# Performance work log

Hardware: AMD Instinct MI355X
Metric: run time of the kernel (lower is better)

Reference implementation:

```python
import jax, jax.numpy as jnp
import numpy as np

NUM_HEADS = 16
THETA = 10000.0


def _rope(x, pos, theta):
    # x: [B, H, S, D], pos: [S] ints. Interleaved-pair RoPE.
    D = x.shape[-1]
    half = D // 2
    inv_freq = theta ** (-(jnp.arange(half, dtype=jnp.float32) * 2.0) / D)  # [half]
    ang = pos.astype(jnp.float32)[:, None] * inv_freq[None, :]              # [S, half]
    cos, sin = jnp.cos(ang), jnp.sin(ang)
    x1 = x[..., 0::2]
    x2 = x[..., 1::2]
    r1 = x1 * cos - x2 * sin
    r2 = x1 * sin + x2 * cos
    return jnp.stack([r1, r2], axis=-1).reshape(x.shape)


def setup_inputs() -> dict:
    key = jax.random.key(0)
    ks = jax.random.split(key, 5)
    B, S, D = 4, 2048, 1024
    scale = 1.0 / np.sqrt(D)
    x = jax.random.normal(ks[0], (B, S, D), dtype=jnp.float32)
    Wq = jax.random.normal(ks[1], (D, D), dtype=jnp.float32) * scale
    Wk = jax.random.normal(ks[2], (D, D), dtype=jnp.float32) * scale
    Wv = jax.random.normal(ks[3], (D, D), dtype=jnp.float32) * scale
    Wo = jax.random.normal(ks[4], (D, D), dtype=jnp.float32) * scale
    token_positions = jnp.arange(S, dtype=jnp.int64)
    return {"x": x, "Wq": Wq, "Wk": Wk, "Wv": Wv, "Wo": Wo,
            "token_positions": token_positions}


def reference(x, Wq, Wk, Wv, Wo, token_positions):
    B, S, D = x.shape
    H = NUM_HEADS
    hd = D // H
    # Projections (weights stored as [d_model, d_k], matching the transposed params)
    q = jnp.einsum('bsd,de->bse', x, Wq).reshape(B, S, H, hd).transpose(0, 2, 1, 3)
    k = jnp.einsum('bsd,de->bse', x, Wk).reshape(B, S, H, hd).transpose(0, 2, 1, 3)
    v = jnp.einsum('bsd,de->bse', x, Wv).reshape(B, S, H, hd).transpose(0, 2, 1, 3)
    # RoPE on q and k
    q = _rope(q, token_positions, THETA)
    k = _rope(k, token_positions, THETA)
    # Causal scaled dot-product attention
    scores = jnp.einsum('bhqd,bhkd->bhqk', q, k) / jnp.sqrt(jnp.float32(hd))
    causal = jnp.tril(jnp.ones((S, S), dtype=bool))
    scores = jnp.where(causal, scores, jnp.float32(-jnp.inf))
    attn = jax.nn.softmax(scores, axis=-1)
    o = jnp.einsum('bhqk,bhkd->bhqd', attn, v)          # [B, H, S, hd]
    o = o.transpose(0, 2, 1, 3).reshape(B, S, D)         # [B, S, D]
    return jnp.einsum('bsd,de->bse', o, Wo)
```

## Files before the change

### kernel.cpp

```cpp
#include <hip/hip_runtime.h>
#include <math.h>

#define B_ 4
#define S_ 2048
#define D_ 1024
#define H_ 16
#define HD_ 64
#define ES_F 0.180336880111f
#define KF (-0.41524101186f)

typedef unsigned short ushort_t;
typedef __attribute__((ext_vector_type(8))) short short8;
typedef __attribute__((ext_vector_type(4))) short short4_t;
typedef __attribute__((ext_vector_type(4))) float f32x4;
typedef __attribute__((ext_vector_type(16))) float f32x16;
typedef __attribute__((ext_vector_type(2))) unsigned uint2v;

typedef const void __attribute__((address_space(1))) gvoid;
typedef void __attribute__((address_space(3))) lvoid;

__device__ __forceinline__ ushort_t f2bf(float f) {
    union { float f; unsigned u; } v; v.f = f;
    unsigned r = (v.u + 0x7FFFu + ((v.u >> 16) & 1u)) >> 16;
    return (ushort_t)r;
}
__device__ __forceinline__ float fexp2(float x) {
#if __has_builtin(__builtin_amdgcn_exp2f)
    return __builtin_amdgcn_exp2f(x);
#else
    return exp2f(x);
#endif
}
__device__ __forceinline__ unsigned pk2t(float a, float b) {
    union { float f; unsigned u; } A, Bv; A.f = a; Bv.f = b;
#if __has_builtin(__builtin_amdgcn_perm)
    return __builtin_amdgcn_perm(Bv.u, A.u, 0x07060302u);
#else
    return (A.u >> 16) | (Bv.u & 0xFFFF0000u);
#endif
}
__device__ __forceinline__ short8 mk_frag(unsigned a, unsigned b, unsigned c, unsigned d) {
    union { unsigned u[4]; short8 s; } t;
    t.u[0] = a; t.u[1] = b; t.u[2] = c; t.u[3] = d; return t.s;
}

__global__ __launch_bounds__(256)
void cvt_all(const float* __restrict__ x, ushort_t* __restrict__ xb,
             const float* __restrict__ W0, const float* __restrict__ W1,
             const float* __restrict__ W2, const float* __restrict__ W3,
             ushort_t* __restrict__ T0, ushort_t* __restrict__ T1,
             ushort_t* __restrict__ T2, ushort_t* __restrict__ T3)
{
    __shared__ __align__(16) float T[64 * 68];
    const int bx = blockIdx.x;
    const int t = threadIdx.x;

    if (bx < 4096) {
        const size_t i = ((size_t)bx * 256 + t) * 8;
        float4 a = *(const float4*)&x[i];
        float4 b = *(const float4*)&x[i + 4];
        short8 o;
        o[0] = (short)f2bf(a.x); o[1] = (short)f2bf(a.y);
        o[2] = (short)f2bf(a.z); o[3] = (short)f2bf(a.w);
        o[4] = (short)f2bf(b.x); o[5] = (short)f2bf(b.y);
        o[6] = (short)f2bf(b.z); o[7] = (short)f2bf(b.w);
        *(short8*)&xb[i] = o;
        return;
    }

    const int id = bx - 4096;
    const int z = id >> 8;
    const float* W = (z == 0) ? W0 : (z == 1) ? W1 : (z == 2) ? W2 : W3;
    ushort_t* Wt = (z == 0) ? T0 : (z == 1) ? T1 : (z == 2) ? T2 : T3;
    const int n0 = (id & 15) * 64, k0 = ((id >> 4) & 15) * 64;

    const int row = t >> 2, c0 = (t & 3) * 16;
#pragma unroll
    for (int u = 0; u < 4; ++u)
        *(float4*)&T[row * 68 + c0 + u * 4] =
            *(const float4*)&W[(size_t)(k0 + row) * D_ + n0 + c0 + u * 4];
    __syncthreads();
    const int n = t >> 2, kc = (t & 3) * 16;
    short8 o0, o1;
#pragma unroll
    for (int kk = 0; kk < 8; ++kk) o0[kk] = (short)f2bf(T[(kc + kk) * 68 + n]);
#pragma unroll
    for (int kk = 0; kk < 8; ++kk) o1[kk] = (short)f2bf(T[(kc + 8 + kk) * 68 + n]);
    *(short8*)&Wt[(size_t)(n0 + n) * D_ + k0 + kc] = o0;
    *(short8*)&Wt[(size_t)(n0 + n) * D_ + k0 + kc + 8] = o1;
}


#define QSTAGE(tt, src, base, dst) {                                           \
    const int kk_ = (tt) * 64;                                                 \
    _Pragma("unroll") for (int i_ = 0; i_ < 4; ++i_) {                         \
        const int rb_ = (i_ * 4 + w) * 8;                                      \
        __builtin_amdgcn_global_load_lds(                                      \
            (gvoid*)&(src)[(size_t)((base) + rb_ + srow) * D_ + kk_ + sch],    \
            (lvoid*)&(dst)[rb_ * 64], 16, 0, 0);                               \
    } }

__global__ __launch_bounds__(256, 2)
void qkv_fused(const ushort_t* __restrict__ A,
               const ushort_t* __restrict__ Wq, const ushort_t* __restrict__ Wk,
               const ushort_t* __restrict__ Wv,
               ushort_t* __restrict__ dQ, ushort_t* __restrict__ dK,
               ushort_t* __restrict__ dV)
{
    __shared__ __align__(16) ushort_t Xs[128 * 64];
    __shared__ __align__(16) ushort_t Qs[128 * 64];
    __shared__ __align__(16) ushort_t Ks[128 * 64];
    __shared__ __align__(16) ushort_t Vs[128 * 64];

    const int tid = threadIdx.x;
    const int lane = tid & 63;
    const int hl = lane >> 5;
    const int lq = lane & 31;
    const int w = tid >> 6;
    const int th = w & 1;
    const int fh = w >> 1;

    const int tokT = blockIdx.x * 128, featT = blockIdx.y * 128;

    const f32x16 zv16 = {0,0,0,0,0,0,0,0,0,0,0,0,0,0,0,0};
    f32x16 accQ[2][2], accK[2][2], accV[2][2];
#pragma unroll
    for (int a = 0; a < 2; ++a)
#pragma unroll
        for (int b = 0; b < 2; ++b) {
            accQ[a][b] = zv16; accK[a][b] = zv16; accV[a][b] = zv16;
        }

    const int srow = lane >> 3;
    const int spc  = lane & 7;
    const int sch  = (spc ^ srow) * 8;

#pragma unroll 1
    for (int t = 0; t < 16; ++t) {
        __syncthreads();
        QSTAGE(t, A,  tokT,  Xs);
        QSTAGE(t, Wq, featT, Qs);
        QSTAGE(t, Wk, featT, Ks);
        QSTAGE(t, Wv, featT, Vs);
        __syncthreads();

#pragma unroll
        for (int ks = 0; ks < 4; ++ks) {
            const int xr = (((ks * 2 + hl) ^ (lq & 7)) << 3);
            short8 xf0 = *(const short8*)&Xs[(th * 64 + lq) * 64 + xr];
            short8 xf1 = *(const short8*)&Xs[(th * 64 + 32 + lq) * 64 + xr];
            short8 qf0 = *(const short8*)&Qs[(fh * 64 + lq) * 64 + xr];
            short8 qf1 = *(const short8*)&Qs[(fh * 64 + 32 + lq) * 64 + xr];
            short8 kf0 = *(const short8*)&Ks[(fh * 64 + lq) * 64 + xr];
            short8 kf1 = *(const short8*)&Ks[(fh * 64 + 32 + lq) * 64 + xr];
            short8 vf0 = *(const short8*)&Vs[(fh * 64 + lq) * 64 + xr];
            short8 vf1 = *(const short8*)&Vs[(fh * 64 + 32 + lq) * 64 + xr];
            accQ[0][0] = __builtin_amdgcn_mfma_f32_32x32x16_bf16(qf0, xf0, accQ[0][0], 0, 0, 0);
            accQ[0][1] = __builtin_amdgcn_mfma_f32_32x32x16_bf16(qf0, xf1, accQ[0][1], 0, 0, 0);
            accQ[1][0] = __builtin_amdgcn_mfma_f32_32x32x16_bf16(qf1, xf0, accQ[1][0], 0, 0, 0);
            accQ[1][1] = __builtin_amdgcn_mfma_f32_32x32x16_bf16(qf1, xf1, accQ[1][1], 0, 0, 0);
            accK[0][0] = __builtin_amdgcn_mfma_f32_32x32x16_bf16(kf0, xf0, accK[0][0], 0, 0, 0);
            accK[0][1] = __builtin_amdgcn_mfma_f32_32x32x16_bf16(kf0, xf1, accK[0][1], 0, 0, 0);
            accK[1][0] = __builtin_amdgcn_mfma_f32_32x32x16_bf16(kf1, xf0, accK[1][0], 0, 0, 0);
            accK[1][1] = __builtin_amdgcn_mfma_f32_32x32x16_bf16(kf1, xf1, accK[1][1], 0, 0, 0);
            accV[0][0] = __builtin_amdgcn_mfma_f32_32x32x16_bf16(xf0, vf0, accV[0][0], 0, 0, 0);
            accV[0][1] = __builtin_amdgcn_mfma_f32_32x32x16_bf16(xf0, vf1, accV[0][1], 0, 0, 0);
            accV[1][0] = __builtin_amdgcn_mfma_f32_32x32x16_bf16(xf1, vf0, accV[1][0], 0, 0, 0);
            accV[1][1] = __builtin_amdgcn_mfma_f32_32x32x16_bf16(xf1, vf1, accV[1][1], 0, 0, 0);
        }
    }

#pragma unroll
    for (int tn = 0; tn < 2; ++tn) {
        const int tok = tokT + th * 64 + tn * 32 + lq;
        const int bb2 = tok >> 11, s0 = tok & (S_ - 1);
        const float fs0 = (float)s0;
#pragma unroll
        for (int tm = 0; tm < 2; ++tm) {
            const int fb = featT + fh * 64 + tm * 32 + 4 * hl;
            const int h = fb >> 6;
            const int ddb = fb & 63;
            ushort_t* dpQ = &dQ[(((size_t)bb2 * H_ + h) * S_ + s0) * HD_];
            ushort_t* dpK = &dK[(((size_t)bb2 * H_ + h) * S_ + s0) * HD_];
#pragma unroll
            for (int g = 0; g < 4; ++g) {
                const int dd = ddb + 8 * g;
                const int jj = dd >> 1;
                const float if0 = exp2f(KF * (float)jj);
                const float if1 = exp2f(KF * (float)(jj + 1));
                float sn0, cs0, sn1, cs1;
                __sincosf(fs0 * if0, &sn0, &cs0);
                __sincosf(fs0 * if1, &sn1, &cs1);
                {
                    const float x0 = accQ[tm][tn][4 * g + 0];
                    const float x1 = accQ[tm][tn][4 * g + 1];
                    const float x2 = accQ[tm][tn][4 * g + 2];
                    const float x3 = accQ[tm][tn][4 * g + 3];
                    short4_t pk;
                    pk[0] = (short)f2bf((x0 * cs0 - x1 * sn0) * ES_F);
                    pk[1] = (short)f2bf((x0 * sn0 + x1 * cs0) * ES_F);
                    pk[2] = (short)f2bf((x2 * cs1 - x3 * sn1) * ES_F);
                    pk[3] = (short)f2bf((x2 * sn1 + x3 * cs1) * ES_F);
                    *(short4_t*)&dpQ[dd] = pk;
                }
                {
                    const float x0 = accK[tm][tn][4 * g + 0];
                    const float x1 = accK[tm][tn][4 * g + 1];
                    const float x2 = accK[tm][tn][4 * g + 2];
                    const float x3 = accK[tm][tn][4 * g + 3];
                    short4_t pk;
                    pk[0] = (short)f2bf(x0 * cs0 - x1 * sn0);
                    pk[1] = (short)f2bf(x0 * sn0 + x1 * cs0);
                    pk[2] = (short)f2bf(x2 * cs1 - x3 * sn1);
                    pk[3] = (short)f2bf(x2 * sn1 + x3 * cs1);
                    *(short4_t*)&dpK[dd] = pk;
                }
            }
        }
    }

#pragma unroll
    for (int tn = 0; tn < 2; ++tn) {
        const int n = featT + fh * 64 + tn * 32 + lq;
        const int h = n >> 6, dd = n & 63;
#pragma unroll
        for (int tm = 0; tm < 2; ++tm) {
            const int mb = tokT + th * 64 + tm * 32 + 4 * hl;
#pragma unroll
            for (int g = 0; g < 4; ++g) {
                const int m_base = mb + 8 * g;
                const int bb2 = m_base >> 11, s0 = m_base & (S_ - 1);
                short4_t pk;
#pragma unroll
                for (int r = 0; r < 4; ++r)
                    pk[r] = (short)f2bf(accV[tm][tn][4 * g + r]);
                *(short4_t*)&dV[(((size_t)bb2 * H_ + h) * HD_ + dd) * S_ + s0] = pk;
            }
        }
    }
}


#define STAGE(tt, Ad, Bd) {                                                    \
    const int kk_ = (tt) * 64;                                                 \
    _Pragma("unroll") for (int i_ = 0; i_ < 4; ++i_) {                         \
        const int rb_ = (i_ * 4 + w) * 8;                                      \
        __builtin_amdgcn_global_load_lds(                                      \
            (gvoid*)&pA[(size_t)(aBase + rb_ + srow) * D_ + kk_ + sch],        \
            (lvoid*)&(Ad)[rb_ * 64], 16, 0, 0);                                \
        __builtin_amdgcn_global_load_lds(                                      \
            (gvoid*)&pB[(size_t)(bBase + rb_ + srow) * D_ + kk_ + sch],        \
            (lvoid*)&(Bd)[rb_ * 64], 16, 0, 0);                                \
    } }

#define COMPUTE(Ab, Bb) {                                                      \
    _Pragma("unroll") for (int ks = 0; ks < 4; ++ks) {                         \
        const int xr_ = (((ks * 2 + hl) ^ (lq & 7)) << 3);                     \
        short8 af0 = *(const short8*)&(Ab)[(wr * 64 + lq) * 64 + xr_];         \
        short8 af1 = *(const short8*)&(Ab)[(wr * 64 + 32 + lq) * 64 + xr_];    \
        short8 bf0 = *(const short8*)&(Bb)[(wc * 64 + lq) * 64 + xr_];         \
        short8 bf1 = *(const short8*)&(Bb)[(wc * 64 + 32 + lq) * 64 + xr_];    \
        acc[0][0] = __builtin_amdgcn_mfma_f32_32x32x16_bf16(af0, bf0, acc[0][0], 0, 0, 0); \
        acc[0][1] = __builtin_amdgcn_mfma_f32_32x32x16_bf16(af0, bf1, acc[0][1], 0, 0, 0); \
        acc[1][0] = __builtin_amdgcn_mfma_f32_32x32x16_bf16(af1, bf0, acc[1][0], 0, 0, 0); \
        acc[1][1] = __builtin_amdgcn_mfma_f32_32x32x16_bf16(af1, bf1, acc[1][1], 0, 0, 0); \
    } }

__global__ __launch_bounds__(256, 2)
void gemm_bt(const ushort_t* __restrict__ A, const ushort_t* __restrict__ W0,
             float* __restrict__ outp)
{
    __shared__ __align__(16) ushort_t As[2 * 128 * 64];
    __shared__ __align__(16) ushort_t Bs[2 * 128 * 64];

    const int tid = threadIdx.x;
    const int lane = tid & 63;
    const int hl = lane >> 5;
    const int lq = lane & 31;
    const int w = tid >> 6, wr = w >> 1, wc = w & 1;

    const int tokT = blockIdx.x * 128, featT = blockIdx.y * 128;
    const ushort_t* pA = A;
    const ushort_t* pB = W0;
    const int aBase = tokT;
    const int bBase = featT;

    const f32x16 zv16 = {0,0,0,0,0,0,0,0,0,0,0,0,0,0,0,0};
    f32x16 acc[2][2];
    acc[0][0] = zv16; acc[0][1] = zv16; acc[1][0] = zv16; acc[1][1] = zv16;

    const int srow = lane >> 3;
    const int spc  = lane & 7;
    const int sch  = (spc ^ srow) * 8;

    ushort_t* A0 = As;  ushort_t* A1 = As + 128 * 64;
    ushort_t* B0 = Bs;  ushort_t* B1 = Bs + 128 * 64;

    STAGE(0, A0, B0);
    __syncthreads();

#pragma unroll 1
    for (int t2 = 0; t2 < 8; ++t2) {
        STAGE(2 * t2 + 1, A1, B1);
        COMPUTE(A0, B0);
        __syncthreads();
        if (t2 < 7) STAGE(2 * t2 + 2, A0, B0);
        COMPUTE(A1, B1);
        __syncthreads();
    }

#pragma unroll
    for (int tn = 0; tn < 2; ++tn) {
        const int n = bBase + wc * 64 + tn * 32 + lq;
#pragma unroll
        for (int tm = 0; tm < 2; ++tm) {
            const int mb = aBase + wr * 64 + tm * 32 + 4 * hl;
#pragma unroll
            for (int g = 0; g < 4; ++g)
#pragma unroll
                for (int r = 0; r < 4; ++r)
                    outp[(size_t)(mb + 8 * g + r) * D_ + n] =
                        acc[tm][tn][4 * g + r];
        }
    }
}

__global__ __launch_bounds__(256)
void attn_mfma(const ushort_t* __restrict__ Q, const ushort_t* __restrict__ K,
               const ushort_t* __restrict__ Vt, ushort_t* __restrict__ O)
{
    __shared__ __align__(16) ushort_t sK[64 * 64];
    __shared__ __align__(16) ushort_t sVt[64 * 64];

    const int tid = threadIdx.x;
    const int lane = tid & 63;
    const int hl = lane >> 5;
    const int lq = lane & 31;
    const int w = tid >> 6;
    const int hb64 = blockIdx.x;
    const int qt = 15 - blockIdx.y;
    const int h = hb64 >> 2, bb = hb64 & 3;
    const size_t hb = ((size_t)(bb * H_ + h)) * S_ * HD_;

    const int srow = lane >> 3;
    const int spc = lane & 7;

    short8 ones;
#pragma unroll
    for (int i = 0; i < 8; ++i) ones[i] = (short)0x3F80;

    const f32x16 zv16 = {0,0,0,0,0,0,0,0,0,0,0,0,0,0,0,0};

    const int q0 = qt * 128;
    const int wq = q0 + w * 32;
    const int qg = wq + lq;

    short8 qf[4];
#pragma unroll
    for (int ks = 0; ks < 4; ++ks)
        qf[ks] = *(const short8*)&Q[hb + (size_t)qg * HD_ + ks * 16 + hl * 8];

    f32x16 oa[2], la;
    oa[0] = zv16; oa[1] = zv16; la = zv16;

    const int nt = q0 / 64 + 2;
    for (int kt = 0; kt < nt; ++kt) {
        const int k0 = kt * 64;
        __syncthreads();
        {
#pragma unroll
            for (int i = 0; i < 2; ++i) {
                const int row = i * 32 + w * 8 + srow;
                const int sc = (spc ^ (row & 7)) * 8;
                __builtin_amdgcn_global_load_lds(
                    (gvoid*)&K[hb + (size_t)(k0 + row) * HD_ + sc],
                    (lvoid*)&sK[(i * 32 + w * 8) * 64], 16, 0, 0);
                __builtin_amdgcn_global_load_lds(
                    (gvoid*)&Vt[hb + (size_t)row * S_ + k0 + sc],
                    (lvoid*)&sVt[(i * 32 + w * 8) * 64], 16, 0, 0);
            }
        }
        __syncthreads();

        if (k0 > wq + 31) continue;

        f32x16 st[2];
        st[0] = zv16; st[1] = zv16;
        const int kr0 = lq, kr1 = 32 + lq;
#pragma unroll
        for (int ks = 0; ks < 4; ++ks) {
            const int ch = ks * 2 + hl;
            short8 ak0 = *(const short8*)&sK[kr0 * 64 + ((ch ^ (kr0 & 7)) << 3)];
            short8 ak1 = *(const short8*)&sK[kr1 * 64 + ((ch ^ (kr1 & 7)) << 3)];
            st[0] = __builtin_amdgcn_mfma_f32_32x32x16_bf16(ak0, qf[ks], st[0], 0, 0, 0);
            st[1] = __builtin_amdgcn_mfma_f32_32x32x16_bf16(ak1, qf[ks], st[1], 0, 0, 0);
        }

        const bool diag = (k0 + 63 > wq);
        short8 pf[4];
#pragma unroll
        for (int nt2 = 0; nt2 < 2; ++nt2) {
            float pv[16];
            const int kb = k0 + nt2 * 32 + 4 * hl;
#pragma unroll
            for (int g = 0; g < 4; ++g)
#pragma unroll
                for (int r = 0; r < 4; ++r) {
                    float s = st[nt2][4 * g + r];
                    if (diag) {
                        const int key = kb + 8 * g + r;
                        s = (key <= qg) ? s : -INFINITY;
                    }
                    pv[4 * g + r] = fexp2(s);
                }
            unsigned P2[8];
#pragma unroll
            for (int g = 0; g < 4; ++g) {
                P2[2 * g]     = pk2t(pv[4 * g + 0], pv[4 * g + 1]);
                P2[2 * g + 1] = pk2t(pv[4 * g + 2], pv[4 * g + 3]);
            }
#if __has_builtin(__builtin_amdgcn_permlane32_swap)
            uint2v r02 = __builtin_amdgcn_permlane32_swap(P2[0], P2[2], false, false);
            uint2v r13 = __builtin_amdgcn_permlane32_swap(P2[1], P2[3], false, false);
            uint2v r46 = __builtin_amdgcn_permlane32_swap(P2[4], P2[6], false, false);
            uint2v r57 = __builtin_amdgcn_permlane32_swap(P2[5], P2[7], false, false);
            pf[nt2 * 2 + 0] = mk_frag(r02[0], r13[0], r02[1], r13[1]);
            pf[nt2 * 2 + 1] = mk_frag(r46[0], r57[0], r46[1], r57[1]);
#else
            unsigned X[8];
#pragma unroll
            for (int m = 0; m < 8; ++m) X[m] = (unsigned)__shfl_xor((int)P2[m], 32);
            pf[nt2 * 2 + 0] = hl ? mk_frag(X[2], X[3], P2[2], P2[3])
                                 : mk_frag(P2[0], P2[1], X[0], X[1]);
            pf[nt2 * 2 + 1] = hl ? mk_frag(X[6], X[7], P2[6], P2[7])
                                 : mk_frag(P2[4], P2[5], X[4], X[5]);
#endif
        }

        const int vr0 = lq, vr1 = 32 + lq;
#pragma unroll
        for (int ks2 = 0; ks2 < 4; ++ks2) {
            const int ch = ks2 * 2 + hl;
            short8 av0 = *(const short8*)&sVt[vr0 * 64 + ((ch ^ (vr0 & 7)) << 3)];
            short8 av1 = *(const short8*)&sVt[vr1 * 64 + ((ch ^ (vr1 & 7)) << 3)];
            oa[0] = __builtin_amdgcn_mfma_f32_32x32x16_bf16(av0, pf[ks2], oa[0], 0, 0, 0);
            oa[1] = __builtin_amdgcn_mfma_f32_32x32x16_bf16(av1, pf[ks2], oa[1], 0, 0, 0);
            la    = __builtin_amdgcn_mfma_f32_32x32x16_bf16(ones, pf[ks2], la, 0, 0, 0);
        }
    }

    const float inv = 1.f / la[0];
    ushort_t* Ob = &O[((size_t)(bb * S_ + qg)) * D_ + h * HD_];
#pragma unroll
    for (int mt = 0; mt < 2; ++mt)
#pragma unroll
        for (int g = 0; g < 4; ++g) {
            short4_t pk;
#pragma unroll
            for (int r = 0; r < 4; ++r)
                pk[r] = (short)f2bf(oa[mt][4 * g + r] * inv);
            *(short4_t*)&Ob[mt * 32 + 8 * g + 4 * hl] = pk;
        }
}

extern "C" void kernel_launch(void* const* d_in, const int* in_sizes, int n_in,
                              void* d_out, int out_size, void* d_ws, size_t ws_size,
                              hipStream_t stream)
{
    (void)in_sizes; (void)n_in; (void)out_size; (void)ws_size;
    const float* x  = (const float*)d_in[0];
    const float* Wq = (const float*)d_in[1];
    const float* Wk = (const float*)d_in[2];
    const float* Wv = (const float*)d_in[3];
    const float* Wo = (const float*)d_in[4];

    float* out = (float*)d_out;
    ushort_t* ws = (ushort_t*)d_ws;
    const size_t NX = (size_t)B_ * S_ * D_;
    const size_t NW = (size_t)D_ * D_;
    ushort_t* xb  = ws;
    ushort_t* Wqt = xb + NX;
    ushort_t* Wkt = Wqt + NW;
    ushort_t* Wvt = Wkt + NW;
    ushort_t* Wot = Wvt + NW;
    ushort_t* Qb  = Wot + NW;
    ushort_t* Kb  = Qb + NX;
    ushort_t* Vtb = Kb + NX;
    ushort_t* Ob  = Vtb + NX;

    cvt_all<<<dim3(4096 + 1024), 256, 0, stream>>>(x, xb, Wq, Wk, Wv, Wo,
                                                   Wqt, Wkt, Wvt, Wot);

    qkv_fused<<<dim3(64, 8), 256, 0, stream>>>(xb, Wqt, Wkt, Wvt, Qb, Kb, Vtb);
    attn_mfma<<<dim3(64, 16), 256, 0, stream>>>(Qb, Kb, Vtb, Ob);
    gemm_bt<<<dim3(64, 8), 256, 0, stream>>>(Ob, Wot, out);
}
```

Before: 242.8 us.

## Split QKV projection tile across eight waves with 512-thread blocks

The fused QKV projection kernel moves from 4 to 8 waves per block. Each wave now computes a 32-feature by 64-token sub-tile instead of 64x64, which halves its accumulator set, and global-to-LDS staging is spread over the larger thread count. The goal is more waves in flight per CU to hide LDS and MFMA latency. In exchange, each MFMA needs relatively more LDS fragment reads, since X fragments are loaded redundantly by more waves. The launch bound of 4 blocks per CU also sets a tight register budget that may force spills, while LDS use (64KB per block) likely caps actual residency below that.

Result: slower. 253.8 us (+4.5%).

```diff
diff --git a/kernel.cpp b/kernel.cpp
--- a/kernel.cpp
+++ b/kernel.cpp
@@ -93,14 +93,14 @@
 
 #define QSTAGE(tt, src, base, dst) {                                           \
     const int kk_ = (tt) * 64;                                                 \
-    _Pragma("unroll") for (int i_ = 0; i_ < 4; ++i_) {                         \
-        const int rb_ = (i_ * 4 + w) * 8;                                      \
+    _Pragma("unroll") for (int i_ = 0; i_ < 2; ++i_) {                         \
+        const int rb_ = (i_ * 8 + w) * 8;                                      \
         __builtin_amdgcn_global_load_lds(                                      \
             (gvoid*)&(src)[(size_t)((base) + rb_ + srow) * D_ + kk_ + sch],    \
             (lvoid*)&(dst)[rb_ * 64], 16, 0, 0);                               \
     } }
 
-__global__ __launch_bounds__(256, 2)
+__global__ __launch_bounds__(512, 4)
 void qkv_fused(const ushort_t* __restrict__ A,
                const ushort_t* __restrict__ Wq, const ushort_t* __restrict__ Wk,
                const ushort_t* __restrict__ Wv,
@@ -123,13 +123,10 @@
     const int tokT = blockIdx.x * 128, featT = blockIdx.y * 128;
 
     const f32x16 zv16 = {0,0,0,0,0,0,0,0,0,0,0,0,0,0,0,0};
-    f32x16 accQ[2][2], accK[2][2], accV[2][2];
-#pragma unroll
-    for (int a = 0; a < 2; ++a)
-#pragma unroll
-        for (int b = 0; b < 2; ++b) {
-            accQ[a][b] = zv16; accK[a][b] = zv16; accV[a][b] = zv16;
-        }
+    f32x16 accQ[2], accK[2], accV[2];
+    accQ[0] = zv16; accQ[1] = zv16;
+    accK[0] = zv16; accK[1] = zv16;
+    accV[0] = zv16; accV[1] = zv16;
 
     const int srow = lane >> 3;
     const int spc  = lane & 7;
@@ -149,37 +146,27 @@
             const int xr = (((ks * 2 + hl) ^ (lq & 7)) << 3);
             short8 xf0 = *(const short8*)&Xs[(th * 64 + lq) * 64 + xr];
             short8 xf1 = *(const short8*)&Xs[(th * 64 + 32 + lq) * 64 + xr];
-            short8 qf0 = *(const short8*)&Qs[(fh * 64 + lq) * 64 + xr];
-            short8 qf1 = *(const short8*)&Qs[(fh * 64 + 32 + lq) * 64 + xr];
-            short8 kf0 = *(const short8*)&Ks[(fh * 64 + lq) * 64 + xr];
-            short8 kf1 = *(const short8*)&Ks[(fh * 64 + 32 + lq) * 64 + xr];
-            short8 vf0 = *(const short8*)&Vs[(fh * 64 + lq) * 64 + xr];
-            short8 vf1 = *(const short8*)&Vs[(fh * 64 + 32 + lq) * 64 + xr];
-            accQ[0][0] = __builtin_amdgcn_mfma_f32_32x32x16_bf16(qf0, xf0, accQ[0][0], 0, 0, 0);
-            accQ[0][1] = __builtin_amdgcn_mfma_f32_32x32x16_bf16(qf0, xf1, accQ[0][1], 0, 0, 0);
-            accQ[1][0] = __builtin_amdgcn_mfma_f32_32x32x16_bf16(qf1, xf0, accQ[1][0], 0, 0, 0);
-            accQ[1][1] = __builtin_amdgcn_mfma_f32_32x32x16_bf16(qf1, xf1, accQ[1][1], 0, 0, 0);
-            accK[0][0] = __builtin_amdgcn_mfma_f32_32x32x16_bf16(kf0, xf0, accK[0][0], 0, 0, 0);
-            accK[0][1] = __builtin_amdgcn_mfma_f32_32x32x16_bf16(kf0, xf1, accK[0][1], 0, 0, 0);
-            accK[1][0] = __builtin_amdgcn_mfma_f32_32x32x16_bf16(kf1, xf0, accK[1][0], 0, 0, 0);
-            accK[1][1] = __builtin_amdgcn_mfma_f32_32x32x16_bf16(kf1, xf1, accK[1][1], 0, 0, 0);
-            accV[0][0] = __builtin_amdgcn_mfma_f32_32x32x16_bf16(xf0, vf0, accV[0][0], 0, 0, 0);
-            accV[0][1] = __builtin_amdgcn_mfma_f32_32x32x16_bf16(xf0, vf1, accV[0][1], 0, 0, 0);
-            accV[1][0] = __builtin_amdgcn_mfma_f32_32x32x16_bf16(xf1, vf0, accV[1][0], 0, 0, 0);
-            accV[1][1] = __builtin_amdgcn_mfma_f32_32x32x16_bf16(xf1, vf1, accV[1][1], 0, 0, 0);
-        }
-    }
-
-#pragma unroll
-    for (int tn = 0; tn < 2; ++tn) {
-        const int tok = tokT + th * 64 + tn * 32 + lq;
-        const int bb2 = tok >> 11, s0 = tok & (S_ - 1);
-        const float fs0 = (float)s0;
-#pragma unroll
-        for (int tm = 0; tm < 2; ++tm) {
-            const int fb = featT + fh * 64 + tm * 32 + 4 * hl;
-            const int h = fb >> 6;
-            const int ddb = fb & 63;
+            short8 qf = *(const short8*)&Qs[(fh * 32 + lq) * 64 + xr];
+            short8 kf = *(const short8*)&Ks[(fh * 32 + lq) * 64 + xr];
+            short8 vf = *(const short8*)&Vs[(fh * 32 + lq) * 64 + xr];
+            accQ[0] = __builtin_amdgcn_mfma_f32_32x32x16_bf16(qf, xf0, accQ[0], 0, 0, 0);
+            accQ[1] = __builtin_amdgcn_mfma_f32_32x32x16_bf16(qf, xf1, accQ[1], 0, 0, 0);
+            accK[0] = __builtin_amdgcn_mfma_f32_32x32x16_bf16(kf, xf0, accK[0], 0, 0, 0);
+            accK[1] = __builtin_amdgcn_mfma_f32_32x32x16_bf16(kf, xf1, accK[1], 0, 0, 0);
+            accV[0] = __builtin_amdgcn_mfma_f32_32x32x16_bf16(xf0, vf, accV[0], 0, 0, 0);
+            accV[1] = __builtin_amdgcn_mfma_f32_32x32x16_bf16(xf1, vf, accV[1], 0, 0, 0);
+        }
+    }
+
+    {
+        const int fb = featT + fh * 32 + 4 * hl;
+        const int h = fb >> 6;
+        const int ddb = fb & 63;
+#pragma unroll
+        for (int tn = 0; tn < 2; ++tn) {
+            const int tok = tokT + th * 64 + tn * 32 + lq;
+            const int bb2 = tok >> 11, s0 = tok & (S_ - 1);
+            const float fs0 = (float)s0;
             ushort_t* dpQ = &dQ[(((size_t)bb2 * H_ + h) * S_ + s0) * HD_];
             ushort_t* dpK = &dK[(((size_t)bb2 * H_ + h) * S_ + s0) * HD_];
 #pragma unroll
@@ -192,10 +179,10 @@
                 __sincosf(fs0 * if0, &sn0, &cs0);
                 __sincosf(fs0 * if1, &sn1, &cs1);
                 {
-                    const float x0 = accQ[tm][tn][4 * g + 0];
-                    const float x1 = accQ[tm][tn][4 * g + 1];
-                    const float x2 = accQ[tm][tn][4 * g + 2];
-                    const float x3 = accQ[tm][tn][4 * g + 3];
+                    const float x0 = accQ[tn][4 * g + 0];
+                    const float x1 = accQ[tn][4 * g + 1];
+                    const float x2 = accQ[tn][4 * g + 2];
+                    const float x3 = accQ[tn][4 * g + 3];
                     short4_t pk;
                     pk[0] = (short)f2bf((x0 * cs0 - x1 * sn0) * ES_F);
                     pk[1] = (short)f2bf((x0 * sn0 + x1 * cs0) * ES_F);
@@ -204,10 +191,10 @@
                     *(short4_t*)&dpQ[dd] = pk;
                 }
                 {
-                    const float x0 = accK[tm][tn][4 * g + 0];
-                    const float x1 = accK[tm][tn][4 * g + 1];
-                    const float x2 = accK[tm][tn][4 * g + 2];
-                    const float x3 = accK[tm][tn][4 * g + 3];
+                    const float x0 = accK[tn][4 * g + 0];
+                    const float x1 = accK[tn][4 * g + 1];
+                    const float x2 = accK[tn][4 * g + 2];
+                    const float x3 = accK[tn][4 * g + 3];
                     short4_t pk;
                     pk[0] = (short)f2bf(x0 * cs0 - x1 * sn0);
                     pk[1] = (short)f2bf(x0 * sn0 + x1 * cs0);
@@ -219,9 +206,8 @@
         }
     }
 
-#pragma unroll
-    for (int tn = 0; tn < 2; ++tn) {
-        const int n = featT + fh * 64 + tn * 32 + lq;
+    {
+        const int n = featT + fh * 32 + lq;
         const int h = n >> 6, dd = n & 63;
 #pragma unroll
         for (int tm = 0; tm < 2; ++tm) {
@@ -233,7 +219,7 @@
                 short4_t pk;
 #pragma unroll
                 for (int r = 0; r < 4; ++r)
-                    pk[r] = (short)f2bf(accV[tm][tn][4 * g + r]);
+                    pk[r] = (short)f2bf(accV[tm][4 * g + r]);
                 *(short4_t*)&dV[(((size_t)bb2 * H_ + h) * HD_ + dd) * S_ + s0] = pk;
             }
         }
@@ -491,7 +477,7 @@
     cvt_all<<<dim3(4096 + 1024), 256, 0, stream>>>(x, xb, Wq, Wk, Wv, Wo,
                                                    Wqt, Wkt, Wvt, Wot);
 
-    qkv_fused<<<dim3(64, 8), 256, 0, stream>>>(xb, Wqt, Wkt, Wvt, Qb, Kb, Vtb);
+    qkv_fused<<<dim3(64, 8), dim3(512), 0, stream>>>(xb, Wqt, Wkt, Wvt, Qb, Kb, Vtb);
     attn_mfma<<<dim3(64, 16), 256, 0, stream>>>(Qb, Kb, Vtb, Ob);
     gemm_bt<<<dim3(64, 8), 256, 0, stream>>>(Ob, Wot, out);
 }
```
